# Kernel optimization log

Hardware: AMD Instinct MI355X
Metric: run time of the kernel (lower is better)

The kernel has to match this reference:

```python
import math
import jax, jax.numpy as jnp
import numpy as np

TAU = 0.07
GROUPS = 8
COST_CH = 96

def _l2norm(x, axis, eps=1e-12):
    # matches torch F.normalize: x / max(||x||_2, eps)
    n = jnp.sqrt(jnp.sum(x * x, axis=axis, keepdims=True))
    return x / jnp.maximum(n, eps)

def setup_inputs() -> dict:
    key = jax.random.key(0)
    k0, k1, k2, k3 = jax.random.split(key, 4)
    B, Cin, H, W = 2, 64, 128, 256
    F_L = jax.random.normal(k0, (B, Cin, H, W), jnp.float32)
    F_R = jax.random.normal(k1, (B, Cin, H, W), jnp.float32)
    WL = jax.random.normal(k2, (COST_CH, Cin), jnp.float32) * 0.1  # pL 1x1 conv weight
    WR = jax.random.normal(k3, (COST_CH, Cin), jnp.float32) * 0.1  # pR 1x1 conv weight
    return {"F_L": F_L, "F_R": F_R, "WL": WL, "WR": WR, "D_orig": 128}

def reference(F_L, F_R, WL, WR, D_orig):
    B, _, H, W = F_L.shape
    Dp = int(math.ceil(D_orig / 4.0))  # Dp_full; full band dmin=0, dmax=Dp-1
    # 1x1 conv projections + channel L2 normalize
    FL = _l2norm(jnp.einsum('bchw,oc->bohw', F_L, WL), axis=1)
    FR = _l2norm(jnp.einsum('bchw,oc->bohw', F_R, WR), axis=1)
    G, Cg = GROUPS, COST_CH // GROUPS
    disp = jnp.arange(Dp)
    # grid_sample(bilinear, border, align_corners=True) with integer disparity
    # shift == border-clamped integer gather along W: x' = clip(x - d, 0, W-1)
    idx = jnp.clip(jnp.arange(W)[None, :] - disp[:, None], 0, W - 1)  # [Dp, W]
    FRs = FR[:, :, :, idx]  # [B, C, H, Dp, W] warped right features
    FLg = FL.reshape(B, G, Cg, H, W)
    FRsg = FRs.reshape(B, G, Cg, H, Dp, W)
    # grouped correlation: reduce over Cg, scaled by 1/sqrt(Cg)
    sim = jnp.einsum('bgchw,bgchdw->bgdhw', FLg, FRsg) / jnp.sqrt(jnp.float32(Cg))
    # sin positional modulation
    psi = jnp.sin(2.0 * jnp.pi * disp.astype(FL.dtype) / max(Dp, 1))
    cost = -(sim + psi[None, None, :, None, None]) / TAU  # [B, G, Dp, H, W]
    return cost
```

## Files before the change

kernel.cpp:

```cpp
#include <hip/hip_runtime.h>
#include <math.h>

#define TAU_F 0.07f
#define B_ 2
#define CIN 64
#define H_ 128
#define W_ 256
#define CC 96
#define G_ 8
#define CG 12
#define DP 32
#define HW_ (H_*W_)
#define ROWF (W_*CG)

__global__ void wtrans_kernel(const float* __restrict__ WL,
                              const float* __restrict__ WR,
                              float* __restrict__ WtL,
                              float* __restrict__ WtR) {
    int i = blockIdx.x * 256 + threadIdx.x;
    if (i >= 2 * CIN * CC) return;
    int side = i / (CIN * CC);
    int r = i % (CIN * CC);
    int c = r / CC;
    int o = r % CC;
    const float* src = side ? WR : WL;
    float* dst = side ? WtR : WtL;
    dst[r] = src[o * CIN + c];
}

__global__ __launch_bounds__(256) void proj_kernel(
    const float* __restrict__ F_L, const float* __restrict__ F_R,
    const float* __restrict__ WtL, const float* __restrict__ WtR,
    float* __restrict__ outL, float* __restrict__ outR)
{
    const int side = blockIdx.y;
    const float* F  = side ? F_R : F_L;
    const float* Wt = side ? WtR : WtL;
    float* out      = side ? outR : outL;

    int p  = blockIdx.x * 256 + threadIdx.x;
    int b  = p / HW_;
    int hw = p % HW_;
    int h  = hw / W_;
    int w  = hw % W_;

    float y[CC];
#pragma unroll
    for (int o = 0; o < CC; ++o) y[o] = 0.f;

    const float* fp = F + (size_t)b * CIN * HW_ + hw;
    for (int c = 0; c < CIN; ++c) {
        float f = fp[(size_t)c * HW_];
        const float* wr = Wt + c * CC;
#pragma unroll
        for (int o = 0; o < CC; ++o) y[o] = fmaf(f, wr[o], y[o]);
    }

    float ss = 0.f;
#pragma unroll
    for (int o = 0; o < CC; ++o) ss = fmaf(y[o], y[o], ss);
    float r = 1.0f / fmaxf(sqrtf(ss), 1e-12f);

    size_t base = (size_t)(b * H_ + h) * (G_ * ROWF);
#pragma unroll
    for (int g = 0; g < G_; ++g) {
#pragma unroll
        for (int j = 0; j < 3; ++j) {
            float4 v;
            v.x = y[g*CG + j*4 + 0] * r;
            v.y = y[g*CG + j*4 + 1] * r;
            v.z = y[g*CG + j*4 + 2] * r;
            v.w = y[g*CG + j*4 + 3] * r;
            *(float4*)&out[base + (size_t)g * ROWF + j * (W_*4) + w * 4] = v;
        }
    }
}

__global__ __launch_bounds__(256) void sim_kernel(
    const float* __restrict__ PL, const float* __restrict__ PR,
    float* __restrict__ out)
{
    __shared__ float flS[ROWF];
    __shared__ float frS[ROWF];
    __shared__ float psiS[DP];

    int blk = blockIdx.x;
    int h = blk % H_;
    int g = (blk / H_) % G_;
    int b = blk / (H_ * G_);
    int tid = threadIdx.x;

    size_t base = ((size_t)(b * H_ + h) * G_ + g) * ROWF;

#pragma unroll
    for (int i = tid; i < ROWF / 4; i += 256) {
        *(float4*)&flS[i * 4] = *(const float4*)&PL[base + (size_t)i * 4];
        *(float4*)&frS[i * 4] = *(const float4*)&PR[base + (size_t)i * 4];
    }
    if (tid < DP)
        psiS[tid] = -sinf(6.28318530717958647692f * (float)tid / (float)DP) / TAU_F;
    __syncthreads();

    const int w = tid;
    float4 fl0 = *(const float4*)&flS[0*1024 + w*4];
    float4 fl1 = *(const float4*)&flS[1*1024 + w*4];
    float4 fl2 = *(const float4*)&flS[2*1024 + w*4];

    const float A = -1.0f / (3.46410161513775459f * TAU_F);
    size_t ob = ((size_t)(b * G_ + g) * DP * H_ + h) * W_ + w;

#pragma unroll
    for (int d = 0; d < DP; ++d) {
        int wd = w - d; if (wd < 0) wd = 0;
        float4 a0 = *(const float4*)&frS[0*1024 + wd*4];
        float4 a1 = *(const float4*)&frS[1*1024 + wd*4];
        float4 a2 = *(const float4*)&frS[2*1024 + wd*4];
        float acc;
        acc = fl0.x * a0.x;
        acc = fmaf(fl0.y, a0.y, acc);
        acc = fmaf(fl0.z, a0.z, acc);
        acc = fmaf(fl0.w, a0.w, acc);
        acc = fmaf(fl1.x, a1.x, acc);
        acc = fmaf(fl1.y, a1.y, acc);
        acc = fmaf(fl1.z, a1.z, acc);
        acc = fmaf(fl1.w, a1.w, acc);
        acc = fmaf(fl2.x, a2.x, acc);
        acc = fmaf(fl2.y, a2.y, acc);
        acc = fmaf(fl2.z, a2.z, acc);
        acc = fmaf(fl2.w, a2.w, acc);
        out[ob + (size_t)d * HW_] = fmaf(acc, A, psiS[d]);
    }
}

extern "C" void kernel_launch(void* const* d_in, const int* in_sizes, int n_in,
                              void* d_out, int out_size, void* d_ws, size_t ws_size,
                              hipStream_t stream) {
    const float* F_L = (const float*)d_in[0];
    const float* F_R = (const float*)d_in[1];
    const float* WL  = (const float*)d_in[2];
    const float* WR  = (const float*)d_in[3];
    float* out = (float*)d_out;
    float* ws  = (float*)d_ws;

    const size_t PROJ = (size_t)B_ * H_ * G_ * ROWF;
    float* PLp = ws;
    float* PRp = ws + PROJ;
    float* WtL = ws + 2 * PROJ;
    float* WtR = WtL + CIN * CC;

    wtrans_kernel<<<(2 * CIN * CC + 255) / 256, 256, 0, stream>>>(WL, WR, WtL, WtR);
    proj_kernel<<<dim3(B_ * HW_ / 256, 2), 256, 0, stream>>>(F_L, F_R, WtL, WtR, PLp, PRp);
    sim_kernel<<<B_ * G_ * H_, 256, 0, stream>>>(PLp, PRp, out);
}
```

Before: 147.1 us.

## Fuse projection, normalization and grouped correlation into one per-row kernel

Merges the projection kernel and the similarity kernel into a single kernel with one 1024-thread block per (batch, row). Each thread computes half of the 96 output channels for one pixel and side, and the two halves are combined through shared memory for the L2 norm. Normalized features go into LDS in two group passes and are correlated there directly. This removes the global round trip of the projected feature maps, but leaves only 256 blocks and makes each thread do heavier projection work.

```diff
diff --git a/kernel.cpp b/kernel.cpp
--- a/kernel.cpp
+++ b/kernel.cpp
@@ -11,7 +11,6 @@
 #define CG 12
 #define DP 32
 #define HW_ (H_*W_)
-#define ROWF (W_*CG)
 
 __global__ void wtrans_kernel(const float* __restrict__ WL,
                               const float* __restrict__ WR,
@@ -28,107 +27,100 @@
     dst[r] = src[o * CIN + c];
 }
 
-__global__ __launch_bounds__(256) void proj_kernel(
+__global__ __launch_bounds__(1024, 4) void fused_kernel(
     const float* __restrict__ F_L, const float* __restrict__ F_R,
     const float* __restrict__ WtL, const float* __restrict__ WtR,
-    float* __restrict__ outL, float* __restrict__ outR)
+    float* __restrict__ out)
 {
-    const int side = blockIdx.y;
+    __shared__ float Sfl[12288];
+    __shared__ float Sfr[12288];
+    __shared__ float ssS[1024];
+    __shared__ float psiS[DP];
+
+    const int t = threadIdx.x;
+    const int b = blockIdx.x >> 7;
+    const int h = blockIdx.x & 127;
+    const int half = t >> 9;
+    const int idx  = t & 511;
+    const int side = idx >> 8;
+    const int w    = idx & 255;
+
+    if (t < DP)
+        psiS[t] = -sinf(6.28318530717958647692f * (float)t / (float)DP) / TAU_F;
+
     const float* F  = side ? F_R : F_L;
     const float* Wt = side ? WtR : WtL;
-    float* out      = side ? outR : outL;
 
-    int p  = blockIdx.x * 256 + threadIdx.x;
-    int b  = p / HW_;
-    int hw = p % HW_;
-    int h  = hw / W_;
-    int w  = hw % W_;
+    float y[48];
+#pragma unroll
+    for (int k = 0; k < 48; ++k) y[k] = 0.f;
 
-    float y[CC];
+    const float* fp = F + (size_t)b * CIN * HW_ + h * W_ + w;
+    for (int c = 0; c < CIN; ++c) {
+        float f = fp[c * HW_];
+        const float* wr = Wt + c * CC + half * 48;
 #pragma unroll
-    for (int o = 0; o < CC; ++o) y[o] = 0.f;
-
-    const float* fp = F + (size_t)b * CIN * HW_ + hw;
-    for (int c = 0; c < CIN; ++c) {
-        float f = fp[(size_t)c * HW_];
-        const float* wr = Wt + c * CC;
-#pragma unroll
-        for (int o = 0; o < CC; ++o) y[o] = fmaf(f, wr[o], y[o]);
+        for (int k = 0; k < 48; ++k) y[k] = fmaf(f, wr[k], y[k]);
     }
 
     float ss = 0.f;
 #pragma unroll
-    for (int o = 0; o < CC; ++o) ss = fmaf(y[o], y[o], ss);
-    float r = 1.0f / fmaxf(sqrtf(ss), 1e-12f);
+    for (int k = 0; k < 48; ++k) ss = fmaf(y[k], y[k], ss);
+    ssS[t] = ss;
+    __syncthreads();
+    float tot = ss + ssS[t ^ 512];
+    float r = 1.0f / fmaxf(sqrtf(tot), 1e-12f);
 
-    size_t base = (size_t)(b * H_ + h) * (G_ * ROWF);
-#pragma unroll
-    for (int g = 0; g < G_; ++g) {
-#pragma unroll
-        for (int j = 0; j < 3; ++j) {
-            float4 v;
-            v.x = y[g*CG + j*4 + 0] * r;
-            v.y = y[g*CG + j*4 + 1] * r;
-            v.z = y[g*CG + j*4 + 2] * r;
-            v.w = y[g*CG + j*4 + 3] * r;
-            *(float4*)&out[base + (size_t)g * ROWF + j * (W_*4) + w * 4] = v;
-        }
-    }
-}
-
-__global__ __launch_bounds__(256) void sim_kernel(
-    const float* __restrict__ PL, const float* __restrict__ PR,
-    float* __restrict__ out)
-{
-    __shared__ float flS[ROWF];
-    __shared__ float frS[ROWF];
-    __shared__ float psiS[DP];
-
-    int blk = blockIdx.x;
-    int h = blk % H_;
-    int g = (blk / H_) % G_;
-    int b = blk / (H_ * G_);
-    int tid = threadIdx.x;
-
-    size_t base = ((size_t)(b * H_ + h) * G_ + g) * ROWF;
+    const int w2 = t & 255;
+    const int gl = (t >> 8) & 3;
+    const float A = -1.0f / (3.46410161513775459f * TAU_F);
 
 #pragma unroll
-    for (int i = tid; i < ROWF / 4; i += 256) {
-        *(float4*)&flS[i * 4] = *(const float4*)&PL[base + (size_t)i * 4];
-        *(float4*)&frS[i * 4] = *(const float4*)&PR[base + (size_t)i * 4];
-    }
-    if (tid < DP)
-        psiS[tid] = -sinf(6.28318530717958647692f * (float)tid / (float)DP) / TAU_F;
-    __syncthreads();
+    for (int p = 0; p < 2; ++p) {
+        if (p) __syncthreads();
+        if (half == p) {
+            float* S = side ? Sfr : Sfl;
+#pragma unroll
+            for (int gq = 0; gq < 4; ++gq) {
+#pragma unroll
+                for (int j = 0; j < 3; ++j) {
+                    float4 v;
+                    v.x = y[gq*12 + j*4 + 0] * r;
+                    v.y = y[gq*12 + j*4 + 1] * r;
+                    v.z = y[gq*12 + j*4 + 2] * r;
+                    v.w = y[gq*12 + j*4 + 3] * r;
+                    *(float4*)&S[((gq*3 + j) * 256 + w) * 4] = v;
+                }
+            }
+        }
+        __syncthreads();
 
-    const int w = tid;
-    float4 fl0 = *(const float4*)&flS[0*1024 + w*4];
-    float4 fl1 = *(const float4*)&flS[1*1024 + w*4];
-    float4 fl2 = *(const float4*)&flS[2*1024 + w*4];
+        const float4 fl0 = *(const float4*)&Sfl[((gl*3 + 0) * 256 + w2) * 4];
+        const float4 fl1 = *(const float4*)&Sfl[((gl*3 + 1) * 256 + w2) * 4];
+        const float4 fl2 = *(const float4*)&Sfl[((gl*3 + 2) * 256 + w2) * 4];
 
-    const float A = -1.0f / (3.46410161513775459f * TAU_F);
-    size_t ob = ((size_t)(b * G_ + g) * DP * H_ + h) * W_ + w;
-
+        size_t ob = (((size_t)(b * G_ + p*4 + gl) * DP) * H_ + h) * (size_t)W_ + w2;
 #pragma unroll
-    for (int d = 0; d < DP; ++d) {
-        int wd = w - d; if (wd < 0) wd = 0;
-        float4 a0 = *(const float4*)&frS[0*1024 + wd*4];
-        float4 a1 = *(const float4*)&frS[1*1024 + wd*4];
-        float4 a2 = *(const float4*)&frS[2*1024 + wd*4];
-        float acc;
-        acc = fl0.x * a0.x;
-        acc = fmaf(fl0.y, a0.y, acc);
-        acc = fmaf(fl0.z, a0.z, acc);
-        acc = fmaf(fl0.w, a0.w, acc);
-        acc = fmaf(fl1.x, a1.x, acc);
-        acc = fmaf(fl1.y, a1.y, acc);
-        acc = fmaf(fl1.z, a1.z, acc);
-        acc = fmaf(fl1.w, a1.w, acc);
-        acc = fmaf(fl2.x, a2.x, acc);
-        acc = fmaf(fl2.y, a2.y, acc);
-        acc = fmaf(fl2.z, a2.z, acc);
-        acc = fmaf(fl2.w, a2.w, acc);
-        out[ob + (size_t)d * HW_] = fmaf(acc, A, psiS[d]);
+        for (int d = 0; d < DP; ++d) {
+            int wd = w2 - d; if (wd < 0) wd = 0;
+            float4 a0 = *(const float4*)&Sfr[((gl*3 + 0) * 256 + wd) * 4];
+            float4 a1 = *(const float4*)&Sfr[((gl*3 + 1) * 256 + wd) * 4];
+            float4 a2 = *(const float4*)&Sfr[((gl*3 + 2) * 256 + wd) * 4];
+            float acc;
+            acc = fl0.x * a0.x;
+            acc = fmaf(fl0.y, a0.y, acc);
+            acc = fmaf(fl0.z, a0.z, acc);
+            acc = fmaf(fl0.w, a0.w, acc);
+            acc = fmaf(fl1.x, a1.x, acc);
+            acc = fmaf(fl1.y, a1.y, acc);
+            acc = fmaf(fl1.z, a1.z, acc);
+            acc = fmaf(fl1.w, a1.w, acc);
+            acc = fmaf(fl2.x, a2.x, acc);
+            acc = fmaf(fl2.y, a2.y, acc);
+            acc = fmaf(fl2.z, a2.z, acc);
+            acc = fmaf(fl2.w, a2.w, acc);
+            out[ob + (size_t)d * HW_] = fmaf(acc, A, psiS[d]);
+        }
     }
 }
 
@@ -142,13 +134,9 @@
     float* out = (float*)d_out;
     float* ws  = (float*)d_ws;
 
-    const size_t PROJ = (size_t)B_ * H_ * G_ * ROWF;
-    float* PLp = ws;
-    float* PRp = ws + PROJ;
-    float* WtL = ws + 2 * PROJ;
-    float* WtR = WtL + CIN * CC;
+    float* WtL = ws;
+    float* WtR = ws + CIN * CC;
 
     wtrans_kernel<<<(2 * CIN * CC + 255) / 256, 256, 0, stream>>>(WL, WR, WtL, WtR);
-    proj_kernel<<<dim3(B_ * HW_ / 256, 2), 256, 0, stream>>>(F_L, F_R, WtL, WtR, PLp, PRp);
-    sim_kernel<<<B_ * G_ * H_, 256, 0, stream>>>(PLp, PRp, out);
+    fused_kernel<<<B_ * H_, 1024, 0, stream>>>(F_L, F_R, WtL, WtR, out);
 }
```

After: 211.3 us. 43.6% more time.

## Split projection output channels across thread halves with LDS-staged inputs

Applied to the files above, without the earlier changes.

The projection kernel now gives each pixel two threads, each computing 48 of the 96 output channels. Input features are staged through shared memory in 16-channel chunks, and the L2 norm is combined across the two halves through shared memory. This cuts per-thread register pressure from 96 accumulators to 48, with launch bounds requesting higher occupancy. The cost is extra barriers and a different block decomposition.

```diff
diff --git a/kernel.cpp b/kernel.cpp
--- a/kernel.cpp
+++ b/kernel.cpp
@@ -28,49 +28,73 @@
     dst[r] = src[o * CIN + c];
 }
 
-__global__ __launch_bounds__(256) void proj_kernel(
+__global__ __launch_bounds__(256, 4) void proj_kernel(
     const float* __restrict__ F_L, const float* __restrict__ F_R,
     const float* __restrict__ WtL, const float* __restrict__ WtR,
     float* __restrict__ outL, float* __restrict__ outR)
 {
-    const int side = blockIdx.y;
+    __shared__ float Fstage[16 * 128];
+    __shared__ float ssS[256];
+
+    const int blk  = blockIdx.x;
+    const int side = blk & 1;
+    const int wh   = (blk >> 1) & 1;
+    const int h    = (blk >> 2) & 127;
+    const int b    = blk >> 9;
+
+    const int t    = threadIdx.x;
+    const int half = t >> 7;
+    const int wl   = t & 127;
+    const int w    = wh * 128 + wl;
+
     const float* F  = side ? F_R : F_L;
     const float* Wt = side ? WtR : WtL;
     float* out      = side ? outR : outL;
 
-    int p  = blockIdx.x * 256 + threadIdx.x;
-    int b  = p / HW_;
-    int hw = p % HW_;
-    int h  = hw / W_;
-    int w  = hw % W_;
+    float y[48];
+#pragma unroll
+    for (int k = 0; k < 48; ++k) y[k] = 0.f;
 
-    float y[CC];
+    const float* fbase = F + (size_t)b * CIN * HW_ + h * W_ + wh * 128;
+
+    for (int cc = 0; cc < 4; ++cc) {
+        {
+            int ci  = t >> 4;
+            int off = (t & 15) * 8;
+            const float* src = fbase + (size_t)(cc * 16 + ci) * HW_ + off;
+            *(float4*)&Fstage[ci * 128 + off]     = *(const float4*)&src[0];
+            *(float4*)&Fstage[ci * 128 + off + 4] = *(const float4*)&src[4];
+        }
+        __syncthreads();
 #pragma unroll
-    for (int o = 0; o < CC; ++o) y[o] = 0.f;
-
-    const float* fp = F + (size_t)b * CIN * HW_ + hw;
-    for (int c = 0; c < CIN; ++c) {
-        float f = fp[(size_t)c * HW_];
-        const float* wr = Wt + c * CC;
+        for (int ci = 0; ci < 16; ++ci) {
+            float f = Fstage[ci * 128 + wl];
+            const float* wr = Wt + (cc * 16 + ci) * CC + half * 48;
 #pragma unroll
-        for (int o = 0; o < CC; ++o) y[o] = fmaf(f, wr[o], y[o]);
+            for (int k = 0; k < 48; ++k) y[k] = fmaf(f, wr[k], y[k]);
+        }
+        __syncthreads();
     }
 
     float ss = 0.f;
 #pragma unroll
-    for (int o = 0; o < CC; ++o) ss = fmaf(y[o], y[o], ss);
-    float r = 1.0f / fmaxf(sqrtf(ss), 1e-12f);
+    for (int k = 0; k < 48; ++k) ss = fmaf(y[k], y[k], ss);
+    ssS[t] = ss;
+    __syncthreads();
+    float tot = ss + ssS[t ^ 128];
+    float r = 1.0f / fmaxf(sqrtf(tot), 1e-12f);
 
     size_t base = (size_t)(b * H_ + h) * (G_ * ROWF);
 #pragma unroll
-    for (int g = 0; g < G_; ++g) {
+    for (int gq = 0; gq < 4; ++gq) {
+        int g = half * 4 + gq;
 #pragma unroll
         for (int j = 0; j < 3; ++j) {
             float4 v;
-            v.x = y[g*CG + j*4 + 0] * r;
-            v.y = y[g*CG + j*4 + 1] * r;
-            v.z = y[g*CG + j*4 + 2] * r;
-            v.w = y[g*CG + j*4 + 3] * r;
+            v.x = y[gq*12 + j*4 + 0] * r;
+            v.y = y[gq*12 + j*4 + 1] * r;
+            v.z = y[gq*12 + j*4 + 2] * r;
+            v.w = y[gq*12 + j*4 + 3] * r;
             *(float4*)&out[base + (size_t)g * ROWF + j * (W_*4) + w * 4] = v;
         }
     }
@@ -149,6 +173,6 @@
     float* WtR = WtL + CIN * CC;
 
     wtrans_kernel<<<(2 * CIN * CC + 255) / 256, 256, 0, stream>>>(WL, WR, WtL, WtR);
-    proj_kernel<<<dim3(B_ * HW_ / 256, 2), 256, 0, stream>>>(F_L, F_R, WtL, WtR, PLp, PRp);
+    proj_kernel<<<dim3(B_ * H_ * 2 * 2), 256, 0, stream>>>(F_L, F_R, WtL, WtR, PLp, PRp);
     sim_kernel<<<B_ * G_ * H_, 256, 0, stream>>>(PLp, PRp, out);
 }
```

New measurement: 207.8 us. +41.3%, slower.
